# Kernel tuning notes

Hardware: AMD Instinct MI355X
Metric: run time of the kernel (lower is better)

## Reference

```python
import jax, jax.numpy as jnp
import numpy as np

EMB_DIM = 256
Q_DIM = 512
V_DIM = 512

def setup_inputs() -> dict:
    key = jax.random.key(0)
    ks = jax.random.split(key, 7)
    B, S = 8, 2048
    x = jax.random.normal(ks[0], (B, S, EMB_DIM), dtype=jnp.float32)
    s = 1.0 / np.sqrt(EMB_DIM)
    Wq = jax.random.normal(ks[1], (EMB_DIM, Q_DIM), dtype=jnp.float32) * s
    bq = jax.random.normal(ks[2], (Q_DIM,), dtype=jnp.float32) * 0.01
    Wk = jax.random.normal(ks[3], (EMB_DIM, Q_DIM), dtype=jnp.float32) * s
    bk = jax.random.normal(ks[4], (Q_DIM,), dtype=jnp.float32) * 0.01
    Wv = jax.random.normal(ks[5], (EMB_DIM, V_DIM), dtype=jnp.float32) * s
    bv = jax.random.normal(ks[6], (V_DIM,), dtype=jnp.float32) * 0.01
    return {"x": x, "Wq": Wq, "bq": bq, "Wk": Wk, "bk": bk, "Wv": Wv, "bv": bv}

def reference(x, Wq, bq, Wk, bk, Wv, bv):
    # q/k/v projections (torch Linear == x @ W + b with W stored [in, out] here)
    q = jax.nn.sigmoid(jnp.einsum('bse,eq->bsq', x, Wq) + bq)   # [B,S,Q]
    k = jnp.einsum('bse,eq->bsq', x, Wk) + bk                   # [B,S,Q]
    v = jnp.einsum('bse,ev->bsv', x, Wv) + bv                   # [B,S,V]
    scale = 1.0 / jnp.sqrt(jnp.float32(EMB_DIM))
    qk = jnp.einsum('bsq,btq->bst', q, k) * scale               # [B,S,S]
    qk = jax.nn.elu(qk)
    attn = jax.nn.softmax(qk, axis=-1)
    return jnp.einsum('bst,btv->bsv', attn, v)                  # [B,S,V]
```

## Files before the change

### kernel.cpp

```cpp
#include <hip/hip_runtime.h>
#include <hip/hip_bf16.h>
#include <math.h>

typedef unsigned short u16;
using short8 = __attribute__((ext_vector_type(8))) short;
using f32x4  = __attribute__((ext_vector_type(4))) float;

#define BK 32


__device__ __forceinline__ u16 f2bf(float f) {
  union { float f; unsigned u; } v; v.f = f;
  unsigned r = v.u + 0x7FFFu + ((v.u >> 16) & 1u);
  return (u16)(r >> 16);
}

__device__ __forceinline__ float fexp(float x) { return __expf(x); }

__device__ __forceinline__ void gld16(const void* g, void* l) {
  __builtin_amdgcn_global_load_lds(
      (const __attribute__((address_space(1))) void*)g,
      (__attribute__((address_space(3))) void*)l,
      16, 0, 0);
}


__device__ __forceinline__ void gemm_core4(const u16* __restrict__ Ag,
                                           const u16* __restrict__ Bg,
                                           int K, int lda, int ldb,
                                           u16* As, u16* Bs,
                                           f32x4 acc[4][4], int w, int l) {
  const int wm = (w & 1) << 6, wn = (w >> 1) << 6;
  const int ln = l & 15, lq = l >> 4;
  const int sr0 = w * 16 + (l >> 2);
  const int sr1 = 64 + sr0;
  const int sk = (l & 3) * 8;

#pragma unroll
  for (int mt = 0; mt < 4; mt++)
#pragma unroll
    for (int nt = 0; nt < 4; nt++) acc[mt][nt] = (f32x4)0.0f;

  for (int k0 = 0; k0 < K; k0 += BK) {
    __syncthreads();
    gld16(Ag + (size_t)sr0 * lda + k0 + sk, As + sr0 * BK + sk);
    gld16(Ag + (size_t)sr1 * lda + k0 + sk, As + sr1 * BK + sk);
    gld16(Bg + (size_t)sr0 * ldb + k0 + sk, Bs + sr0 * BK + sk);
    gld16(Bg + (size_t)sr1 * ldb + k0 + sk, Bs + sr1 * BK + sk);
    __syncthreads();
    short8 af[4], bf[4];
#pragma unroll
    for (int mt = 0; mt < 4; mt++)
      af[mt] = *(const short8*)(As + (wm + mt * 16 + ln) * BK + lq * 8);
#pragma unroll
    for (int nt = 0; nt < 4; nt++)
      bf[nt] = *(const short8*)(Bs + (wn + nt * 16 + ln) * BK + lq * 8);
#pragma unroll
    for (int mt = 0; mt < 4; mt++)
#pragma unroll
      for (int nt = 0; nt < 4; nt++)
        acc[mt][nt] = __builtin_amdgcn_mfma_f32_16x16x32_bf16(
            af[mt], bf[nt], acc[mt][nt], 0, 0, 0);
  }
}


__global__ __launch_bounds__(256) void k_convx(const float* __restrict__ x,
                                               u16* __restrict__ xb, int n4) {
  int i = blockIdx.x * 256 + threadIdx.x;
  if (i < n4) {
    float4 v = ((const float4*)x)[i];
    ushort4 o;
    o.x = f2bf(v.x); o.y = f2bf(v.y); o.z = f2bf(v.z); o.w = f2bf(v.w);
    ((ushort4*)xb)[i] = o;
  }
}

__global__ __launch_bounds__(256) void k_convw(
    const float* __restrict__ Wq, const float* __restrict__ Wk,
    const float* __restrict__ Wv, const float* __restrict__ bq,
    const float* __restrict__ bk, const float* __restrict__ bv,
    u16* __restrict__ Wt, float* __restrict__ bcat) {
  int i = blockIdx.x * 256 + threadIdx.x;
  if (i < 1536 * 256) {
    int nn = i >> 8, e = i & 255;
    int sel = nn >> 9, c = nn & 511;
    const float* W = (sel == 0) ? Wq : (sel == 1) ? Wk : Wv;
    Wt[i] = f2bf(W[e * 512 + c]);
    if (e == 0) {
      const float* bb = (sel == 0) ? bq : (sel == 1) ? bk : bv;
      bcat[nn] = bb[c];
    }
  }
}


__global__ __launch_bounds__(256) void k_proj(
    const u16* __restrict__ xb, const u16* __restrict__ Wt,
    const float* __restrict__ bcat, u16* __restrict__ qb,
    u16* __restrict__ kb, u16* __restrict__ vb) {
  __shared__ __align__(16) u16 As[128 * BK];
  __shared__ __align__(16) u16 Bs[128 * BK];
  const int bm = blockIdx.y * 128, bn = blockIdx.x * 128;
  const int tid = threadIdx.x, w = tid >> 6, l = tid & 63;
  f32x4 acc[4][4];
  gemm_core4(xb + (size_t)bm * 256, Wt + (size_t)bn * 256, 256, 256, 256,
             As, Bs, acc, w, l);

  const int wm = (w & 1) << 6, wn = (w >> 1) << 6;
  const int ln = l & 15, lq = l >> 4;
  const int sel = blockIdx.x >> 2;
  u16* dst = (sel == 0) ? qb : (sel == 1) ? kb : vb;
  const int cb = (blockIdx.x & 3) * 128;
#pragma unroll
  for (int mt = 0; mt < 4; mt++)
#pragma unroll
    for (int r = 0; r < 4; r++) {
      int row = bm + wm + mt * 16 + lq * 4 + r;
#pragma unroll
      for (int nt = 0; nt < 4; nt++) {
        int col = wn + nt * 16 + ln;
        float v = acc[mt][nt][r] + bcat[bn + col];
        float ov = (sel == 0) ? __builtin_amdgcn_rcpf(1.0f + fexp(-v)) : v;
        dst[(size_t)row * 512 + cb + col] = f2bf(ov);
      }
    }
}


__global__ __launch_bounds__(256) void k_transv(const u16* __restrict__ vb,
                                                u16* __restrict__ vtb) {
  const int b = blockIdx.z;
  const int t0 = blockIdx.y * 64, v0 = blockIdx.x * 64;
  __shared__ u16 tl[64][68];
  const u16* src = vb + (size_t)b * 2048 * 512;
  u16* dst = vtb + (size_t)b * 512 * 2048;
  for (int i = threadIdx.x; i < 1024; i += 256) {
    int r = i >> 4, c4 = (i & 15) * 4;
    *(ushort4*)&tl[r][c4] =
        *(const ushort4*)&src[(size_t)(t0 + r) * 512 + v0 + c4];
  }
  __syncthreads();
  for (int i = threadIdx.x; i < 1024; i += 256) {
    int r = i >> 4, c4 = (i & 15) * 4;
    ushort4 o;
    o.x = tl[c4 + 0][r]; o.y = tl[c4 + 1][r];
    o.z = tl[c4 + 2][r]; o.w = tl[c4 + 3][r];
    *(ushort4*)&dst[(size_t)(v0 + r) * 2048 + t0 + c4] = o;
  }
}


__global__ __launch_bounds__(256) void k_qk(const u16* __restrict__ qb,
                                            const u16* __restrict__ kb,
                                            u16* __restrict__ P,
                                            float* __restrict__ lsum) {
  __shared__ __align__(16) u16 As[128 * BK];
  __shared__ __align__(16) u16 Bs[128 * BK];
  const int b = blockIdx.z;
  const int bm = blockIdx.y * 128, bn = blockIdx.x * 128;
  const size_t ob = (size_t)b * 2048 * 512;
  const int tid = threadIdx.x, w = tid >> 6, l = tid & 63;
  f32x4 acc[4][4];
  gemm_core4(qb + ob + (size_t)bm * 512, kb + ob + (size_t)bn * 512,
             512, 512, 512, As, Bs, acc, w, l);

  const int wm = (w & 1) << 6, wn = (w >> 1) << 6;
  const int ln = l & 15, lq = l >> 4;
  const float scale = 0.0625f;
#pragma unroll
  for (int mt = 0; mt < 4; mt++)
#pragma unroll
    for (int r = 0; r < 4; r++) {
      int row = bm + wm + mt * 16 + lq * 4 + r;
      float s = 0.0f;
#pragma unroll
      for (int nt = 0; nt < 4; nt++) {
        int col = bn + wn + nt * 16 + ln;
        float v = acc[mt][nt][r] * scale;
        float e = (v > 0.0f) ? v : (fexp(v) - 1.0f);
        float p = fexp(e);
        P[((size_t)b * 2048 + row) * 2048 + col] = f2bf(p);
        s += p;
      }
#pragma unroll
      for (int o = 1; o < 16; o <<= 1) s += __shfl_xor(s, o);
      if (ln == 0) atomicAdd(&lsum[b * 2048 + row], s);
    }
}


__global__ __launch_bounds__(512, 4) void k_pv(const u16* __restrict__ P,
                                               const u16* __restrict__ vtb,
                                               const float* __restrict__ lsum,
                                               float* __restrict__ out) {
  __shared__ __align__(16) u16 smem[16384];
  const int b = blockIdx.z;
  const int bm = blockIdx.y * 128, bn = blockIdx.x * 128;
  const int tid = threadIdx.x;
  const int g = tid >> 8;
  const int t = tid & 255;
  const int w = t >> 6, l = t & 63;
  u16* As = smem + g * 8192;
  u16* Bs = smem + g * 8192 + 4096;

  f32x4 acc[4][4];
  gemm_core4(P  + (size_t)b * 2048 * 2048 + (size_t)bm * 2048 + g * 1024,
             vtb + (size_t)b * 512 * 2048 + (size_t)bn * 2048 + g * 1024,
             1024, 2048, 2048, As, Bs, acc, w, l);

  f32x4* red = (f32x4*)smem;
#pragma unroll
  for (int half = 0; half < 2; half++) {
    __syncthreads();
    if (g == 1) {
#pragma unroll
      for (int m2 = 0; m2 < 2; m2++)
#pragma unroll
        for (int nt = 0; nt < 4; nt++)
          red[((m2 * 4 + nt) * 4 + w) * 64 + l] = acc[half * 2 + m2][nt];
    }
    __syncthreads();
    if (g == 0) {
#pragma unroll
      for (int m2 = 0; m2 < 2; m2++)
#pragma unroll
        for (int nt = 0; nt < 4; nt++)
          acc[half * 2 + m2][nt] += red[((m2 * 4 + nt) * 4 + w) * 64 + l];
    }
  }

  if (g == 0) {
    const int wm = (w & 1) << 6, wn = (w >> 1) << 6;
    const int ln = l & 15, lq = l >> 4;
#pragma unroll
    for (int mt = 0; mt < 4; mt++)
#pragma unroll
      for (int r = 0; r < 4; r++) {
        int row = bm + wm + mt * 16 + lq * 4 + r;
        float inv = 1.0f / lsum[b * 2048 + row];
#pragma unroll
        for (int nt = 0; nt < 4; nt++) {
          int col = bn + wn + nt * 16 + ln;
          out[((size_t)b * 2048 + row) * 512 + col] = acc[mt][nt][r] * inv;
        }
      }
  }
}


extern "C" void kernel_launch(void* const* d_in, const int* in_sizes, int n_in,
                              void* d_out, int out_size, void* d_ws, size_t ws_size,
                              hipStream_t stream) {
  const float* x  = (const float*)d_in[0];
  const float* Wq = (const float*)d_in[1];
  const float* bq = (const float*)d_in[2];
  const float* Wk = (const float*)d_in[3];
  const float* bk = (const float*)d_in[4];
  const float* Wv = (const float*)d_in[5];
  const float* bv = (const float*)d_in[6];
  float* out = (float*)d_out;
  char* ws = (char*)d_ws;

  u16*  qb   = (u16*)(ws + 0);
  u16*  kb   = (u16*)(ws + 16777216);
  u16*  vtb  = (u16*)(ws + 33554432);
  float* lsum = (float*)(ws + 50331648);
  u16*  P    = (u16*)(ws + 50397184);
  u16*  xb   = (u16*)(ws + 50397184);
  u16*  Wt   = (u16*)(ws + 58785792);
  float* bcat = (float*)(ws + 59572224);
  u16*  vb   = (u16*)(ws + 59578368);

  k_convx<<<4096, 256, 0, stream>>>(x, xb, 16384 * 256 / 4);
  k_convw<<<1536, 256, 0, stream>>>(Wq, Wk, Wv, bq, bk, bv, Wt, bcat);
  k_proj<<<dim3(12, 128, 1), 256, 0, stream>>>(xb, Wt, bcat, qb, kb, vb);
  k_transv<<<dim3(8, 32, 8), 256, 0, stream>>>(vb, vtb);
  hipMemsetAsync(lsum, 0, 16384 * sizeof(float), stream);
  k_qk<<<dim3(16, 16, 8), 256, 0, stream>>>(qb, kb, P, lsum);
  k_pv<<<dim3(4, 16, 8), 512, 0, stream>>>(P, vtb, lsum, out);
}
```

Before: 238.4 us.

## Fuse V transpose into projection epilogue, merge conversions, simplify PV kernel

```diff
diff --git a/kernel.cpp b/kernel.cpp
--- a/kernel.cpp
+++ b/kernel.cpp
@@ -65,24 +65,21 @@
 }
 
 
-__global__ __launch_bounds__(256) void k_convx(const float* __restrict__ x,
-                                               u16* __restrict__ xb, int n4) {
-  int i = blockIdx.x * 256 + threadIdx.x;
-  if (i < n4) {
+__global__ __launch_bounds__(256) void k_conv(
+    const float* __restrict__ x, u16* __restrict__ xb,
+    const float* __restrict__ Wq, const float* __restrict__ Wk,
+    const float* __restrict__ Wv, const float* __restrict__ bq,
+    const float* __restrict__ bk, const float* __restrict__ bv,
+    u16* __restrict__ Wt, float* __restrict__ bcat) {
+  const int bid = blockIdx.x;
+  if (bid < 4096) {
+    int i = bid * 256 + threadIdx.x;
     float4 v = ((const float4*)x)[i];
     ushort4 o;
     o.x = f2bf(v.x); o.y = f2bf(v.y); o.z = f2bf(v.z); o.w = f2bf(v.w);
     ((ushort4*)xb)[i] = o;
-  }
-}
-
-__global__ __launch_bounds__(256) void k_convw(
-    const float* __restrict__ Wq, const float* __restrict__ Wk,
-    const float* __restrict__ Wv, const float* __restrict__ bq,
-    const float* __restrict__ bk, const float* __restrict__ bv,
-    u16* __restrict__ Wt, float* __restrict__ bcat) {
-  int i = blockIdx.x * 256 + threadIdx.x;
-  if (i < 1536 * 256) {
+  } else {
+    int i = (bid - 4096) * 256 + threadIdx.x;
     int nn = i >> 8, e = i & 255;
     int sel = nn >> 9, c = nn & 511;
     const float* W = (sel == 0) ? Wq : (sel == 1) ? Wk : Wv;
@@ -98,9 +95,10 @@
 __global__ __launch_bounds__(256) void k_proj(
     const u16* __restrict__ xb, const u16* __restrict__ Wt,
     const float* __restrict__ bcat, u16* __restrict__ qb,
-    u16* __restrict__ kb, u16* __restrict__ vb) {
-  __shared__ __align__(16) u16 As[128 * BK];
-  __shared__ __align__(16) u16 Bs[128 * BK];
+    u16* __restrict__ kb, u16* __restrict__ vtb) {
+  __shared__ __align__(16) u16 smem[8704];
+  u16* As = smem;
+  u16* Bs = smem + 4096;
   const int bm = blockIdx.y * 128, bn = blockIdx.x * 128;
   const int tid = threadIdx.x, w = tid >> 6, l = tid & 63;
   f32x4 acc[4][4];
@@ -110,51 +108,61 @@
   const int wm = (w & 1) << 6, wn = (w >> 1) << 6;
   const int ln = l & 15, lq = l >> 4;
   const int sel = blockIdx.x >> 2;
-  u16* dst = (sel == 0) ? qb : (sel == 1) ? kb : vb;
   const int cb = (blockIdx.x & 3) * 128;
-#pragma unroll
-  for (int mt = 0; mt < 4; mt++)
-#pragma unroll
-    for (int r = 0; r < 4; r++) {
-      int row = bm + wm + mt * 16 + lq * 4 + r;
-#pragma unroll
-      for (int nt = 0; nt < 4; nt++) {
-        int col = wn + nt * 16 + ln;
-        float v = acc[mt][nt][r] + bcat[bn + col];
-        float ov = (sel == 0) ? __builtin_amdgcn_rcpf(1.0f + fexp(-v)) : v;
-        dst[(size_t)row * 512 + cb + col] = f2bf(ov);
-      }
-    }
-}
-
-
-__global__ __launch_bounds__(256) void k_transv(const u16* __restrict__ vb,
-                                                u16* __restrict__ vtb) {
-  const int b = blockIdx.z;
-  const int t0 = blockIdx.y * 64, v0 = blockIdx.x * 64;
-  __shared__ u16 tl[64][68];
-  const u16* src = vb + (size_t)b * 2048 * 512;
-  u16* dst = vtb + (size_t)b * 512 * 2048;
-  for (int i = threadIdx.x; i < 1024; i += 256) {
-    int r = i >> 4, c4 = (i & 15) * 4;
-    *(ushort4*)&tl[r][c4] =
-        *(const ushort4*)&src[(size_t)(t0 + r) * 512 + v0 + c4];
+
+  if (sel < 2) {
+    u16* dst = sel ? kb : qb;
+#pragma unroll
+    for (int mt = 0; mt < 4; mt++)
+#pragma unroll
+      for (int r = 0; r < 4; r++) {
+        int row = bm + wm + mt * 16 + lq * 4 + r;
+#pragma unroll
+        for (int nt = 0; nt < 4; nt++) {
+          int col = wn + nt * 16 + ln;
+          float v = acc[mt][nt][r] + bcat[bn + col];
+          float ov = (sel == 0) ? __builtin_amdgcn_rcpf(1.0f + fexp(-v)) : v;
+          dst[(size_t)row * 512 + cb + col] = f2bf(ov);
+        }
+      }
+  } else {
+    const int b = bm >> 11, t0 = bm & 2047;
+#pragma unroll
+    for (int h = 0; h < 2; h++) {
+      __syncthreads();
+      if ((w & 1) == h) {
+#pragma unroll
+        for (int mt = 0; mt < 4; mt++)
+#pragma unroll
+          for (int nt = 0; nt < 4; nt++) {
+            int c = wn + nt * 16 + ln;
+            float bias = bcat[bn + c];
+#pragma unroll
+            for (int r = 0; r < 4; r++) {
+              int lr = mt * 16 + lq * 4 + r;
+              smem[c * 68 + lr] = f2bf(acc[mt][nt][r] + bias);
+            }
+          }
+      }
+      __syncthreads();
+      int c2 = tid >> 1, half = tid & 1;
+      size_t dbase = ((size_t)b * 512 + cb + c2) * 2048 + t0 + h * 64 + half * 32;
+#pragma unroll
+      for (int j = 0; j < 4; j++) {
+        ushort4 a0 = *(const ushort4*)&smem[c2 * 68 + half * 32 + j * 8];
+        ushort4 a1 = *(const ushort4*)&smem[c2 * 68 + half * 32 + j * 8 + 4];
+        *(ushort4*)&vtb[dbase + j * 8] = a0;
+        *(ushort4*)&vtb[dbase + j * 8 + 4] = a1;
+      }
+    }
   }
-  __syncthreads();
-  for (int i = threadIdx.x; i < 1024; i += 256) {
-    int r = i >> 4, c4 = (i & 15) * 4;
-    ushort4 o;
-    o.x = tl[c4 + 0][r]; o.y = tl[c4 + 1][r];
-    o.z = tl[c4 + 2][r]; o.w = tl[c4 + 3][r];
-    *(ushort4*)&dst[(size_t)(v0 + r) * 2048 + t0 + c4] = o;
-  }
-}
-
-
-__global__ __launch_bounds__(256) void k_qk(const u16* __restrict__ qb,
-                                            const u16* __restrict__ kb,
-                                            u16* __restrict__ P,
-                                            float* __restrict__ lsum) {
+}
+
+
+__global__ __launch_bounds__(256, 4) void k_qk(const u16* __restrict__ qb,
+                                               const u16* __restrict__ kb,
+                                               u16* __restrict__ P,
+                                               float* __restrict__ lsum) {
   __shared__ __align__(16) u16 As[128 * BK];
   __shared__ __align__(16) u16 Bs[128 * BK];
   const int b = blockIdx.z;
@@ -190,62 +198,34 @@
 }
 
 
-__global__ __launch_bounds__(512, 4) void k_pv(const u16* __restrict__ P,
-                                               const u16* __restrict__ vtb,
-                                               const float* __restrict__ lsum,
-                                               float* __restrict__ out) {
-  __shared__ __align__(16) u16 smem[16384];
+__global__ __launch_bounds__(256) void k_pv(const u16* __restrict__ P,
+                                            const u16* __restrict__ vtb,
+                                            const float* __restrict__ lsum,
+                                            float* __restrict__ out) {
+  __shared__ __align__(16) u16 As[128 * BK];
+  __shared__ __align__(16) u16 Bs[128 * BK];
   const int b = blockIdx.z;
   const int bm = blockIdx.y * 128, bn = blockIdx.x * 128;
-  const int tid = threadIdx.x;
-  const int g = tid >> 8;
-  const int t = tid & 255;
-  const int w = t >> 6, l = t & 63;
-  u16* As = smem + g * 8192;
-  u16* Bs = smem + g * 8192 + 4096;
-
+  const int tid = threadIdx.x, w = tid >> 6, l = tid & 63;
   f32x4 acc[4][4];
-  gemm_core4(P  + (size_t)b * 2048 * 2048 + (size_t)bm * 2048 + g * 1024,
-             vtb + (size_t)b * 512 * 2048 + (size_t)bn * 2048 + g * 1024,
-             1024, 2048, 2048, As, Bs, acc, w, l);
-
-  f32x4* red = (f32x4*)smem;
-#pragma unroll
-  for (int half = 0; half < 2; half++) {
-    __syncthreads();
-    if (g == 1) {
-#pragma unroll
-      for (int m2 = 0; m2 < 2; m2++)
-#pragma unroll
-        for (int nt = 0; nt < 4; nt++)
-          red[((m2 * 4 + nt) * 4 + w) * 64 + l] = acc[half * 2 + m2][nt];
-    }
-    __syncthreads();
-    if (g == 0) {
-#pragma unroll
-      for (int m2 = 0; m2 < 2; m2++)
-#pragma unroll
-        for (int nt = 0; nt < 4; nt++)
-          acc[half * 2 + m2][nt] += red[((m2 * 4 + nt) * 4 + w) * 64 + l];
-    }
-  }
-
-  if (g == 0) {
-    const int wm = (w & 1) << 6, wn = (w >> 1) << 6;
-    const int ln = l & 15, lq = l >> 4;
-#pragma unroll
-    for (int mt = 0; mt < 4; mt++)
-#pragma unroll
-      for (int r = 0; r < 4; r++) {
-        int row = bm + wm + mt * 16 + lq * 4 + r;
-        float inv = 1.0f / lsum[b * 2048 + row];
-#pragma unroll
-        for (int nt = 0; nt < 4; nt++) {
-          int col = bn + wn + nt * 16 + ln;
-          out[((size_t)b * 2048 + row) * 512 + col] = acc[mt][nt][r] * inv;
-        }
-      }
-  }
+  gemm_core4(P  + (size_t)b * 2048 * 2048 + (size_t)bm * 2048,
+             vtb + (size_t)b * 512 * 2048 + (size_t)bn * 2048,
+             2048, 2048, 2048, As, Bs, acc, w, l);
+
+  const int wm = (w & 1) << 6, wn = (w >> 1) << 6;
+  const int ln = l & 15, lq = l >> 4;
+#pragma unroll
+  for (int mt = 0; mt < 4; mt++)
+#pragma unroll
+    for (int r = 0; r < 4; r++) {
+      int row = bm + wm + mt * 16 + lq * 4 + r;
+      float inv = 1.0f / lsum[b * 2048 + row];
+#pragma unroll
+      for (int nt = 0; nt < 4; nt++) {
+        int col = bn + wn + nt * 16 + ln;
+        out[((size_t)b * 2048 + row) * 512 + col] = acc[mt][nt][r] * inv;
+      }
+    }
 }
 
 
@@ -270,13 +250,10 @@
   u16*  xb   = (u16*)(ws + 50397184);
   u16*  Wt   = (u16*)(ws + 58785792);
   float* bcat = (float*)(ws + 59572224);
-  u16*  vb   = (u16*)(ws + 59578368);
-
-  k_convx<<<4096, 256, 0, stream>>>(x, xb, 16384 * 256 / 4);
-  k_convw<<<1536, 256, 0, stream>>>(Wq, Wk, Wv, bq, bk, bv, Wt, bcat);
-  k_proj<<<dim3(12, 128, 1), 256, 0, stream>>>(xb, Wt, bcat, qb, kb, vb);
-  k_transv<<<dim3(8, 32, 8), 256, 0, stream>>>(vb, vtb);
+
+  k_conv<<<5632, 256, 0, stream>>>(x, xb, Wq, Wk, Wv, bq, bk, bv, Wt, bcat);
+  k_proj<<<dim3(12, 128, 1), 256, 0, stream>>>(xb, Wt, bcat, qb, kb, vtb);
   hipMemsetAsync(lsum, 0, 16384 * sizeof(float), stream);
   k_qk<<<dim3(16, 16, 8), 256, 0, stream>>>(qb, kb, P, lsum);
-  k_pv<<<dim3(4, 16, 8), 512, 0, stream>>>(P, vtb, lsum, out);
-}
+  k_pv<<<dim3(4, 16, 8), 256, 0, stream>>>(P, vtb, lsum, out);
+}
```

Result: faster. 228.5 us (-4.1%).
